# Kernel tuning notes

Measured on AMD Instinct MI355X. Metric: run time of the kernel, lower is better.

The kernel has to match this reference:

```python
import jax, jax.numpy as jnp
import numpy as np

B, T, D, H = 2, 2048, 2048, 32
HD = D // H
# quantization scales (constructor-time attributes in the original repo)
A_PROJ = 3e-4   # q/k/v proj alpha (W8A8B8O8Linear)
A_QK = 2e-5     # qk_bmm alpha (BMM_S8T_S8N_F32T)
A_PV = 1e-2     # pv_bmm alpha (BMM_S8T_S8N_S8T)
A_OUT = 1e-4    # out_proj alpha (W8A8BFP32OFP32Linear)


def _i8(key, shape):
    return jax.random.randint(key, shape, -128, 128, dtype=jnp.int32).astype(jnp.int8)


def setup_inputs() -> dict:
    key = jax.random.key(0)
    ks = jax.random.split(key, 10)
    hidden_states = _i8(ks[0], (B, T, D))
    # causal mask, 0 on/below diagonal, large negative above
    causal = jnp.triu(jnp.full((T, T), -1e9, dtype=jnp.float32), k=1)
    attention_mask = jnp.broadcast_to(causal, (B, 1, T, T))
    return {
        "hidden_states": hidden_states,
        "attention_mask": attention_mask,
        "Wq": _i8(ks[1], (D, D)), "bq": _i8(ks[2], (D,)),
        "Wk": _i8(ks[3], (D, D)), "bk": _i8(ks[4], (D,)),
        "Wv": _i8(ks[5], (D, D)), "bv": _i8(ks[6], (D,)),
        "Wo": _i8(ks[7], (D, D)),
        "bo": jax.random.normal(ks[8], (D,), dtype=jnp.float32),
    }


def _w8a8b8o8(x_i8, W_i8, b_i8, alpha):
    # int8 GEMM -> int32 accum; epilogue: alpha*acc + bias, saturate to int8
    acc = jnp.einsum('btk,nk->btn', x_i8.astype(jnp.int32), W_i8.astype(jnp.int32))
    y = alpha * acc.astype(jnp.float32) + b_i8.astype(jnp.float32)
    return jnp.clip(jnp.round(y), -128, 127).astype(jnp.int8)


def reference(hidden_states, attention_mask, Wq, bq, Wk, bk, Wv, bv, Wo, bo):
    # q/k/v projections: int8 in, int8 out
    q = _w8a8b8o8(hidden_states, Wq, bq, A_PROJ)
    k = _w8a8b8o8(hidden_states, Wk, bk, A_PROJ)
    v = _w8a8b8o8(hidden_states, Wv, bv, A_PROJ)

    def shape(x):  # [B,T,D] -> [B,H,T,HD]
        return x.reshape(B, T, H, HD).transpose(0, 2, 1, 3)

    qh, kh, vh = shape(q), shape(k), shape(v)

    # qk_bmm (BMM_S8T_S8N_F32T): fp32 = alpha * int8 q @ k^T
    attn = A_QK * jnp.einsum('bhtd,bhsd->bhts',
                             qh.astype(jnp.int32), kh.astype(jnp.int32)).astype(jnp.float32)
    attn = attn + attention_mask  # [B,1,T,T] broadcasts over heads
    attn = jnp.maximum(attn, jnp.finfo(jnp.float32).min)
    probs = jax.nn.softmax(attn, axis=-1)

    # quantize probs: p.mul_(127).round_() -> int8
    p_i8 = jnp.clip(jnp.round(probs * 127.0), -128, 127).astype(jnp.int8)

    # pv_bmm (BMM_S8T_S8N_S8T): int8 out = sat(round(alpha * p @ v))
    pv = jnp.einsum('bhts,bhsd->bhtd', p_i8.astype(jnp.int32), vh.astype(jnp.int32))
    attn_out_i8 = jnp.clip(jnp.round(A_PV * pv.astype(jnp.float32)), -128, 127).astype(jnp.int8)

    # [B,H,T,HD] -> [B,T,D]
    attn_out = attn_out_i8.transpose(0, 2, 1, 3).reshape(B, T, D)

    # out_proj (W8A8BFP32OFP32Linear): fp32 = alpha*(x@W^T) + fp32 bias
    acc = jnp.einsum('btk,nk->btn', attn_out.astype(jnp.int32), Wo.astype(jnp.int32))
    out = A_OUT * acc.astype(jnp.float32) + bo
    return out
```

## Files before the change

kernel.cpp:

```cpp
#include <hip/hip_runtime.h>
#include <cstdint>

#define A_PROJ 3e-4f
#define A_QK   2e-5f
#define A_PV   1e-2f
#define A_OUT  1e-4f

#define NB 2
#define NT 2048
#define ND 2048
#define NH 32
#define NHD 64
#define NM (NB*NT)

typedef int v4i __attribute__((ext_vector_type(4)));

__device__ __forceinline__ int8_t sat8(float y) {
  float r = rintf(y);
  r = fminf(fmaxf(r, -128.f), 127.f);
  return (int8_t)(int)r;
}

__device__ __forceinline__ float exp2_fast(float x) {
  return __builtin_amdgcn_exp2f(x);
}

__device__ __forceinline__ void gl2lds16(const int8_t* g, int8_t* l) {
  __builtin_amdgcn_global_load_lds(
      (const __attribute__((address_space(1))) void*)g,
      (__attribute__((address_space(3))) void*)l, 16, 0, 0);
}

#define NWW (ND*ND/4)
__global__ void pack_all(const int* __restrict__ X,
                         const int* __restrict__ W0, const int* __restrict__ W1,
                         const int* __restrict__ W2, const int* __restrict__ W3,
                         int8_t* __restrict__ dX, int8_t* __restrict__ dW0,
                         int8_t* __restrict__ dW1, int8_t* __restrict__ dW2,
                         int8_t* __restrict__ dW3) {
  int i = blockIdx.x * blockDim.x + threadIdx.x;
  const int nx = NM*ND/4;
  const int* src; int8_t* dst; int off;
  if (i < nx) { src = X; dst = dX; off = i; }
  else {
    int j = i - nx;
    int r = j >> 20;
    off = j & (NWW - 1);
    src = (r == 0) ? W0 : (r == 1) ? W1 : (r == 2) ? W2 : W3;
    dst = (r == 0) ? dW0 : (r == 1) ? dW1 : (r == 2) ? dW2 : dW3;
  }
  int4 v = ((const int4*)src)[off];
  uint32_t p = (uint32_t)(v.x & 255) | ((uint32_t)(v.y & 255) << 8) |
               ((uint32_t)(v.z & 255) << 16) | ((uint32_t)(v.w & 255) << 24);
  ((uint32_t*)dst)[off] = p;
}

__global__ __launch_bounds__(256) void gemm_qkv(
    const int8_t* __restrict__ X,
    const int8_t* __restrict__ Wq, const int8_t* __restrict__ Wk, const int8_t* __restrict__ Wv,
    const int* __restrict__ bq, const int* __restrict__ bk, const int* __restrict__ bv,
    int8_t* __restrict__ Qh, int8_t* __restrict__ Kh, int8_t* __restrict__ Vt)
{
  __shared__ __align__(16) int8_t As[2][128][64];
  __shared__ __align__(16) int8_t Bs[2][128][64];
  const int z = blockIdx.z;
  const int8_t* W  = (z == 0) ? Wq : ((z == 1) ? Wk : Wv);
  const int* bias  = (z == 0) ? bq : ((z == 1) ? bk : bv);
  const int m0 = blockIdx.x * 128, n0 = blockIdx.y * 128;
  const int tid = threadIdx.x, lane = tid & 63, wave = tid >> 6;
  const int wm = wave >> 1, wn = wave & 1;
  const int l15 = lane & 15, quad = lane >> 4;

  const int srow = lane >> 2;
  const int scol = (((lane & 3) ^ ((lane >> 3) & 3)) * 16);
  const int rqcol = (quad ^ ((l15 >> 1) & 3)) * 16;

  v4i acc[4][4];
  const v4i vzero = {0, 0, 0, 0};
  #pragma unroll
  for (int i = 0; i < 4; ++i)
    #pragma unroll
    for (int j = 0; j < 4; ++j) acc[i][j] = vzero;

  for (int k0 = 0; k0 < ND; k0 += 128) {
    #pragma unroll
    for (int j = 0; j < 8; ++j) {
      int slot = j * 4 + wave;
      int sl = slot & 15;
      int hh = sl >> 3, rblk = sl & 7;
      int row = rblk * 16 + srow;
      if (slot < 16) {
        gl2lds16(&X[(size_t)(m0 + row) * ND + k0 + hh * 64 + scol], &As[hh][rblk * 16][0]);
      } else {
        gl2lds16(&W[(size_t)(n0 + row) * ND + k0 + hh * 64 + scol], &Bs[hh][rblk * 16][0]);
      }
    }
    __syncthreads();
    #pragma unroll
    for (int hh = 0; hh < 2; ++hh) {
      v4i a[4], b[4];
      #pragma unroll
      for (int mt = 0; mt < 4; ++mt) a[mt] = *(const v4i*)&As[hh][wm*64 + mt*16 + l15][rqcol];
      #pragma unroll
      for (int nt = 0; nt < 4; ++nt) b[nt] = *(const v4i*)&Bs[hh][wn*64 + nt*16 + l15][rqcol];
      #pragma unroll
      for (int mt = 0; mt < 4; ++mt)
        #pragma unroll
        for (int nt = 0; nt < 4; ++nt)
          acc[mt][nt] = __builtin_amdgcn_mfma_i32_16x16x64_i8(a[mt], b[nt], acc[mt][nt], 0, 0, 0);
    }
    __syncthreads();
  }

  float bf[4];
  #pragma unroll
  for (int nt = 0; nt < 4; ++nt) bf[nt] = (float)bias[n0 + wn*64 + nt*16 + l15];

  #pragma unroll
  for (int mt = 0; mt < 4; ++mt)
    #pragma unroll
    for (int nt = 0; nt < 4; ++nt)
      #pragma unroll
      for (int r = 0; r < 4; ++r) {
        int m = m0 + wm*64 + mt*16 + quad*4 + r;
        int n = n0 + wn*64 + nt*16 + l15;
        int8_t q = sat8(A_PROJ * (float)acc[mt][nt][r] + bf[nt]);
        int bb = m >> 11, t = m & (NT - 1);
        int hd8 = n >> 6, hd = n & (NHD - 1);
        size_t bh = (size_t)bb * NH + hd8;
        if (z == 2) Vt[(bh * NHD + hd) * NT + t] = q;
        else ((z == 0) ? Qh : Kh)[(bh * NT + t) * NHD + hd] = q;
      }
}

__global__ __launch_bounds__(256) void attn_fused(
    const int8_t* __restrict__ Qh, const int8_t* __restrict__ Kh, const int8_t* __restrict__ Vt,
    int8_t* __restrict__ AO)
{
  __shared__ __align__(16) int8_t Ks[128][64];
  __shared__ __align__(16) int8_t Vs[64][128];
  __shared__ __align__(16) uint32_t Ps32[4][16][36];

  const int bx = blockIdx.x;
  const int bh = blockIdx.y;
  const int tid = threadIdx.x, lane = tid & 63, wave = tid >> 6;
  const int l15 = lane & 15, quad = lane >> 4;
  const v4i vzero = {0, 0, 0, 0};
  const float MAGIC = 12582912.0f;
  const float C2 = 2.8853900817779268e-05f;

  const int8_t* Qp = Qh + (size_t)bh * NT * NHD;
  const int8_t* Kp = Kh + (size_t)bh * NT * NHD;
  const int8_t* Vp = Vt + (size_t)bh * NHD * NT;
  const int bb = bh >> 5, hhead = bh & (NH - 1);

  const int kst_row = lane >> 2;
  const int kst_col = (((lane & 3) ^ ((lane >> 3) & 3)) * 16);
  const int vst_row = lane >> 3;
  const int vst_col = (((lane & 7) ^ ((lane >> 3) & 7)) * 16);
  const int kfcol = (quad ^ ((l15 >> 1) & 3)) * 16;

  for (int half = 0; half < 2; ++half) {
    const int xq = half ? (31 - bx) : bx;
    const int t0 = xq * 64;
    const int sd = xq >> 1;
    const int tme = t0 + wave * 16 + l15;

    v4i qf = *(const v4i*)&Qp[(size_t)(t0 + wave * 16 + l15) * NHD + quad * 16];

    float lsum = 0.f;
    for (int st = 0; st <= sd; ++st) {
      const int s0 = st * 128;
      #pragma unroll
      for (int j = 0; j < 2; ++j)
        gl2lds16(&Kp[(size_t)(s0 + j*64 + wave*16 + kst_row) * NHD + kst_col],
                 &Ks[j*64 + wave*16][0]);
      __syncthreads();
      v4i kf[8];
      #pragma unroll
      for (int mt = 0; mt < 8; ++mt) kf[mt] = *(const v4i*)&Ks[mt*16 + l15][kfcol];
      if (st < sd) {
        #pragma unroll
        for (int mt = 0; mt < 8; ++mt) {
          v4i sa = __builtin_amdgcn_mfma_i32_16x16x64_i8(kf[mt], qf, vzero, 0, 0, 0);
          #pragma unroll
          for (int r = 0; r < 4; ++r) lsum += exp2_fast(C2 * (float)sa[r]);
        }
      } else {
        #pragma unroll
        for (int mt = 0; mt < 8; ++mt) {
          v4i sa = __builtin_amdgcn_mfma_i32_16x16x64_i8(kf[mt], qf, vzero, 0, 0, 0);
          const int sbase = s0 + mt*16 + quad*4;
          #pragma unroll
          for (int r = 0; r < 4; ++r) {
            float e = exp2_fast(C2 * (float)sa[r]);
            lsum += (sbase + r <= tme) ? e : 0.f;
          }
        }
      }
      __syncthreads();
    }
    {
      lsum += __shfl_xor(lsum, 16, 64);
      lsum += __shfl_xor(lsum, 32, 64);
    }
    const float linv = 127.0f / lsum;

    v4i accv[4];
    #pragma unroll
    for (int j = 0; j < 4; ++j) accv[j] = vzero;

    for (int st = 0; st <= sd; ++st) {
      const int s0 = st * 128;
      #pragma unroll
      for (int j = 0; j < 2; ++j)
        gl2lds16(&Kp[(size_t)(s0 + j*64 + wave*16 + kst_row) * NHD + kst_col],
                 &Ks[j*64 + wave*16][0]);
      #pragma unroll
      for (int j = 0; j < 2; ++j)
        gl2lds16(&Vp[(size_t)(j*32 + wave*8 + vst_row) * NT + s0 + vst_col],
                 &Vs[j*32 + wave*8][0]);
      __syncthreads();
      v4i kf[8];
      #pragma unroll
      for (int mt = 0; mt < 8; ++mt) kf[mt] = *(const v4i*)&Ks[mt*16 + l15][kfcol];

      if (st < sd) {
        #pragma unroll
        for (int mt = 0; mt < 8; ++mt) {
          v4i sa = __builtin_amdgcn_mfma_i32_16x16x64_i8(kf[mt], qf, vzero, 0, 0, 0);
          uint32_t pk = 0;
          #pragma unroll
          for (int r = 0; r < 4; ++r) {
            float e = exp2_fast(C2 * (float)sa[r]);
            float f = fmaf(e, linv, MAGIC);
            pk |= (__float_as_uint(f) & 0xFFu) << (8 * r);
          }
          Ps32[wave][l15][mt*4 + quad] = pk;
        }
      } else {
        #pragma unroll
        for (int mt = 0; mt < 8; ++mt) {
          v4i sa = __builtin_amdgcn_mfma_i32_16x16x64_i8(kf[mt], qf, vzero, 0, 0, 0);
          uint32_t pk = 0;
          const int sbase = s0 + mt*16 + quad*4;
          #pragma unroll
          for (int r = 0; r < 4; ++r) {
            float e = (sbase + r <= tme) ? exp2_fast(C2 * (float)sa[r]) : 0.f;
            float f = fmaf(e, linv, MAGIC);
            pk |= (__float_as_uint(f) & 0xFFu) << (8 * r);
          }
          Ps32[wave][l15][mt*4 + quad] = pk;
        }
      }
      #pragma unroll
      for (int ks = 0; ks < 2; ++ks) {
        v4i ap = *(const v4i*)&Ps32[wave][l15][ks*16 + quad*4];
        #pragma unroll
        for (int nt2 = 0; nt2 < 4; ++nt2) {
          v4i bv = *(const v4i*)&Vs[nt2*16 + l15][(((ks*4 + quad) ^ (l15 & 7)) * 16)];
          accv[nt2] = __builtin_amdgcn_mfma_i32_16x16x64_i8(ap, bv, accv[nt2], 0, 0, 0);
        }
      }
      __syncthreads();
    }

    #pragma unroll
    for (int nt2 = 0; nt2 < 4; ++nt2)
      #pragma unroll
      for (int r = 0; r < 4; ++r) {
        int t = t0 + wave*16 + quad*4 + r;
        int d = nt2*16 + l15;
        AO[((size_t)bb * NT + t) * ND + hhead * NHD + d] = sat8(A_PV * (float)accv[nt2][r]);
      }
  }
}

__global__ __launch_bounds__(256) void gemm_out(
    const int8_t* __restrict__ X, const int8_t* __restrict__ W,
    const float* __restrict__ bo, float* __restrict__ out)
{
  __shared__ __align__(16) int8_t As[2][128][64];
  __shared__ __align__(16) int8_t Bs[2][128][64];
  const int m0 = blockIdx.x * 128, n0 = blockIdx.y * 128;
  const int tid = threadIdx.x, lane = tid & 63, wave = tid >> 6;
  const int wm = wave >> 1, wn = wave & 1;
  const int l15 = lane & 15, quad = lane >> 4;
  const int srow = lane >> 2;
  const int scol = (((lane & 3) ^ ((lane >> 3) & 3)) * 16);
  const int rqcol = (quad ^ ((l15 >> 1) & 3)) * 16;

  v4i acc[4][4];
  const v4i vzero = {0, 0, 0, 0};
  #pragma unroll
  for (int i = 0; i < 4; ++i)
    #pragma unroll
    for (int j = 0; j < 4; ++j) acc[i][j] = vzero;

  for (int k0 = 0; k0 < ND; k0 += 128) {
    #pragma unroll
    for (int j = 0; j < 8; ++j) {
      int slot = j * 4 + wave;
      int sl = slot & 15;
      int hh = sl >> 3, rblk = sl & 7;
      int row = rblk * 16 + srow;
      if (slot < 16) {
        gl2lds16(&X[(size_t)(m0 + row) * ND + k0 + hh * 64 + scol], &As[hh][rblk * 16][0]);
      } else {
        gl2lds16(&W[(size_t)(n0 + row) * ND + k0 + hh * 64 + scol], &Bs[hh][rblk * 16][0]);
      }
    }
    __syncthreads();
    #pragma unroll
    for (int hh = 0; hh < 2; ++hh) {
      v4i a[4], b[4];
      #pragma unroll
      for (int mt = 0; mt < 4; ++mt) a[mt] = *(const v4i*)&As[hh][wm*64 + mt*16 + l15][rqcol];
      #pragma unroll
      for (int nt = 0; nt < 4; ++nt) b[nt] = *(const v4i*)&Bs[hh][wn*64 + nt*16 + l15][rqcol];
      #pragma unroll
      for (int mt = 0; mt < 4; ++mt)
        #pragma unroll
        for (int nt = 0; nt < 4; ++nt)
          acc[mt][nt] = __builtin_amdgcn_mfma_i32_16x16x64_i8(a[mt], b[nt], acc[mt][nt], 0, 0, 0);
    }
    __syncthreads();
  }

  float bf[4];
  #pragma unroll
  for (int nt = 0; nt < 4; ++nt) bf[nt] = bo[n0 + wn*64 + nt*16 + l15];

  #pragma unroll
  for (int mt = 0; mt < 4; ++mt)
    #pragma unroll
    for (int nt = 0; nt < 4; ++nt)
      #pragma unroll
      for (int r = 0; r < 4; ++r) {
        int m = m0 + wm*64 + mt*16 + quad*4 + r;
        int n = n0 + wn*64 + nt*16 + l15;
        out[(size_t)m * ND + n] = A_OUT * (float)acc[mt][nt][r] + bf[nt];
      }
}

extern "C" void kernel_launch(void* const* d_in, const int* in_sizes, int n_in,
                              void* d_out, int out_size, void* d_ws, size_t ws_size,
                              hipStream_t stream)
{
  const int*   hs  = (const int*)d_in[0];
  const int*   Wq  = (const int*)d_in[2];
  const int*   bq  = (const int*)d_in[3];
  const int*   Wk  = (const int*)d_in[4];
  const int*   bkb = (const int*)d_in[5];
  const int*   Wv  = (const int*)d_in[6];
  const int*   bvb = (const int*)d_in[7];
  const int*   Wo  = (const int*)d_in[8];
  const float* bo  = (const float*)d_in[9];
  float* out = (float*)d_out;

  char* ws = (char*)d_ws;
  const size_t SZ_X = (size_t)NM * ND;
  const size_t SZ_W = (size_t)ND * ND;
  const size_t SZ_H = (size_t)NB * NH * NT * NHD;
  int8_t* Xp  = (int8_t*)ws;
  int8_t* Wqp = (int8_t*)(ws + SZ_X);
  int8_t* Wkp = Wqp + SZ_W;
  int8_t* Wvp = Wkp + SZ_W;
  int8_t* Wop = Wvp + SZ_W;
  int8_t* Qh  = Wop + SZ_W;
  int8_t* Kh  = Qh + SZ_H;
  int8_t* Vt  = Kh + SZ_H;
  int8_t* AO  = Xp;

  const int ntot = (int)(SZ_X/4 + 4 * (SZ_W/4));
  pack_all<<<(ntot + 255) / 256, 256, 0, stream>>>(hs, Wq, Wk, Wv, Wo,
                                                   Xp, Wqp, Wkp, Wvp, Wop);

  gemm_qkv<<<dim3(NM/128, ND/128, 3), 256, 0, stream>>>(Xp, Wqp, Wkp, Wvp, bq, bkb, bvb, Qh, Kh, Vt);
  attn_fused<<<dim3(16, NB*NH), 256, 0, stream>>>(Qh, Kh, Vt, AO);
  gemm_out<<<dim3(NM/128, ND/128), 256, 0, stream>>>(AO, Wop, bo, out);
}
```

Baseline: 336.2 us.

## Load GEMM B operand directly to registers and double-buffer A tile in LDS

New measurement: 389.2 us. 1.16x slower.

```diff
diff --git a/kernel.cpp b/kernel.cpp
--- a/kernel.cpp
+++ b/kernel.cpp
@@ -55,14 +55,13 @@
   ((uint32_t*)dst)[off] = p;
 }
 
-__global__ __launch_bounds__(256) void gemm_qkv(
+__global__ __launch_bounds__(256, 3) void gemm_qkv(
     const int8_t* __restrict__ X,
     const int8_t* __restrict__ Wq, const int8_t* __restrict__ Wk, const int8_t* __restrict__ Wv,
     const int* __restrict__ bq, const int* __restrict__ bk, const int* __restrict__ bv,
     int8_t* __restrict__ Qh, int8_t* __restrict__ Kh, int8_t* __restrict__ Vt)
 {
   __shared__ __align__(16) int8_t As[2][128][64];
-  __shared__ __align__(16) int8_t Bs[2][128][64];
   const int z = blockIdx.z;
   const int8_t* W  = (z == 0) ? Wq : ((z == 1) ? Wk : Wv);
   const int* bias  = (z == 0) ? bq : ((z == 1) ? bk : bv);
@@ -75,6 +74,13 @@
   const int scol = (((lane & 3) ^ ((lane >> 3) & 3)) * 16);
   const int rqcol = (quad ^ ((l15 >> 1) & 3)) * 16;
 
+  const int8_t* Xa0 = X + (size_t)(m0 + wave * 16 + srow) * ND + scol;
+  const int8_t* Xa1 = X + (size_t)(m0 + (wave + 4) * 16 + srow) * ND + scol;
+  int8_t* lA0[2] = { &As[0][wave * 16][0], &As[1][wave * 16][0] };
+  int8_t* lA1[2] = { &As[0][(wave + 4) * 16][0], &As[1][(wave + 4) * 16][0] };
+
+  const int8_t* Wb = W + (size_t)(n0 + wn * 64 + l15) * ND + quad * 16;
+
   v4i acc[4][4];
   const v4i vzero = {0, 0, 0, 0};
   #pragma unroll
@@ -82,55 +88,86 @@
     #pragma unroll
     for (int j = 0; j < 4; ++j) acc[i][j] = vzero;
 
+  v4i bcur[4], bnxt[4];
+  gl2lds16(Xa0, lA0[0]);
+  gl2lds16(Xa1, lA1[0]);
+  #pragma unroll
+  for (int nt = 0; nt < 4; ++nt) bcur[nt] = *(const v4i*)(Wb + (size_t)nt * 16 * ND);
+
   for (int k0 = 0; k0 < ND; k0 += 128) {
-    #pragma unroll
-    for (int j = 0; j < 8; ++j) {
-      int slot = j * 4 + wave;
-      int sl = slot & 15;
-      int hh = sl >> 3, rblk = sl & 7;
-      int row = rblk * 16 + srow;
-      if (slot < 16) {
-        gl2lds16(&X[(size_t)(m0 + row) * ND + k0 + hh * 64 + scol], &As[hh][rblk * 16][0]);
-      } else {
-        gl2lds16(&W[(size_t)(n0 + row) * ND + k0 + hh * 64 + scol], &Bs[hh][rblk * 16][0]);
-      }
-    }
     __syncthreads();
-    #pragma unroll
-    for (int hh = 0; hh < 2; ++hh) {
-      v4i a[4], b[4];
-      #pragma unroll
-      for (int mt = 0; mt < 4; ++mt) a[mt] = *(const v4i*)&As[hh][wm*64 + mt*16 + l15][rqcol];
-      #pragma unroll
-      for (int nt = 0; nt < 4; ++nt) b[nt] = *(const v4i*)&Bs[hh][wn*64 + nt*16 + l15][rqcol];
+    gl2lds16(Xa0 + k0 + 64, lA0[1]);
+    gl2lds16(Xa1 + k0 + 64, lA1[1]);
+    #pragma unroll
+    for (int nt = 0; nt < 4; ++nt) bnxt[nt] = *(const v4i*)(Wb + (size_t)nt * 16 * ND + k0 + 64);
+    {
+      v4i a[4];
+      #pragma unroll
+      for (int mt = 0; mt < 4; ++mt) a[mt] = *(const v4i*)&As[0][wm*64 + mt*16 + l15][rqcol];
       #pragma unroll
       for (int mt = 0; mt < 4; ++mt)
         #pragma unroll
         for (int nt = 0; nt < 4; ++nt)
-          acc[mt][nt] = __builtin_amdgcn_mfma_i32_16x16x64_i8(a[mt], b[nt], acc[mt][nt], 0, 0, 0);
+          acc[mt][nt] = __builtin_amdgcn_mfma_i32_16x16x64_i8(a[mt], bcur[nt], acc[mt][nt], 0, 0, 0);
     }
     __syncthreads();
+    if (k0 + 128 < ND) {
+      gl2lds16(Xa0 + k0 + 128, lA0[0]);
+      gl2lds16(Xa1 + k0 + 128, lA1[0]);
+      #pragma unroll
+      for (int nt = 0; nt < 4; ++nt) bcur[nt] = *(const v4i*)(Wb + (size_t)nt * 16 * ND + k0 + 128);
+    }
+    {
+      v4i a[4];
+      #pragma unroll
+      for (int mt = 0; mt < 4; ++mt) a[mt] = *(const v4i*)&As[1][wm*64 + mt*16 + l15][rqcol];
+      #pragma unroll
+      for (int mt = 0; mt < 4; ++mt)
+        #pragma unroll
+        for (int nt = 0; nt < 4; ++nt)
+          acc[mt][nt] = __builtin_amdgcn_mfma_i32_16x16x64_i8(a[mt], bnxt[nt], acc[mt][nt], 0, 0, 0);
+    }
   }
 
   float bf[4];
   #pragma unroll
   for (int nt = 0; nt < 4; ++nt) bf[nt] = (float)bias[n0 + wn*64 + nt*16 + l15];
 
-  #pragma unroll
-  for (int mt = 0; mt < 4; ++mt)
-    #pragma unroll
-    for (int nt = 0; nt < 4; ++nt)
-      #pragma unroll
-      for (int r = 0; r < 4; ++r) {
-        int m = m0 + wm*64 + mt*16 + quad*4 + r;
+  if (z == 2) {
+    #pragma unroll
+    for (int mt = 0; mt < 4; ++mt)
+      #pragma unroll
+      for (int nt = 0; nt < 4; ++nt) {
+        int tbase = (m0 + wm*64 + mt*16 + quad*4) & (NT - 1);
+        int bb = (m0 + wm*64) >> 11;
         int n = n0 + wn*64 + nt*16 + l15;
-        int8_t q = sat8(A_PROJ * (float)acc[mt][nt][r] + bf[nt]);
-        int bb = m >> 11, t = m & (NT - 1);
-        int hd8 = n >> 6, hd = n & (NHD - 1);
-        size_t bh = (size_t)bb * NH + hd8;
-        if (z == 2) Vt[(bh * NHD + hd) * NT + t] = q;
-        else ((z == 0) ? Qh : Kh)[(bh * NT + t) * NHD + hd] = q;
-      }
+        int hh = n >> 6, hd = n & (NHD - 1);
+        uint32_t pk = 0;
+        #pragma unroll
+        for (int r = 0; r < 4; ++r) {
+          uint32_t q = (uint32_t)(uint8_t)sat8(A_PROJ * (float)acc[mt][nt][r] + bf[nt]);
+          pk |= q << (8 * r);
+        }
+        size_t bh = (size_t)bb * NH + hh;
+        *(uint32_t*)&Vt[(bh * NHD + hd) * NT + tbase] = pk;
+      }
+  } else {
+    int8_t* O = (z == 0) ? Qh : Kh;
+    #pragma unroll
+    for (int mt = 0; mt < 4; ++mt)
+      #pragma unroll
+      for (int nt = 0; nt < 4; ++nt)
+        #pragma unroll
+        for (int r = 0; r < 4; ++r) {
+          int m = m0 + wm*64 + mt*16 + quad*4 + r;
+          int n = n0 + wn*64 + nt*16 + l15;
+          int8_t q = sat8(A_PROJ * (float)acc[mt][nt][r] + bf[nt]);
+          int bb = m >> 11, t = m & (NT - 1);
+          int hh = n >> 6, hd = n & (NHD - 1);
+          size_t bh = (size_t)bb * NH + hh;
+          O[(bh * NT + t) * NHD + hd] = q;
+        }
+  }
 }
 
 __global__ __launch_bounds__(256) void attn_fused(
@@ -276,12 +313,11 @@
   }
 }
 
-__global__ __launch_bounds__(256) void gemm_out(
+__global__ __launch_bounds__(256, 3) void gemm_out(
     const int8_t* __restrict__ X, const int8_t* __restrict__ W,
     const float* __restrict__ bo, float* __restrict__ out)
 {
   __shared__ __align__(16) int8_t As[2][128][64];
-  __shared__ __align__(16) int8_t Bs[2][128][64];
   const int m0 = blockIdx.x * 128, n0 = blockIdx.y * 128;
   const int tid = threadIdx.x, lane = tid & 63, wave = tid >> 6;
   const int wm = wave >> 1, wn = wave & 1;
@@ -290,6 +326,12 @@
   const int scol = (((lane & 3) ^ ((lane >> 3) & 3)) * 16);
   const int rqcol = (quad ^ ((l15 >> 1) & 3)) * 16;
 
+  const int8_t* Xa0 = X + (size_t)(m0 + wave * 16 + srow) * ND + scol;
+  const int8_t* Xa1 = X + (size_t)(m0 + (wave + 4) * 16 + srow) * ND + scol;
+  int8_t* lA0[2] = { &As[0][wave * 16][0], &As[1][wave * 16][0] };
+  int8_t* lA1[2] = { &As[0][(wave + 4) * 16][0], &As[1][(wave + 4) * 16][0] };
+  const int8_t* Wb = W + (size_t)(n0 + wn * 64 + l15) * ND + quad * 16;
+
   v4i acc[4][4];
   const v4i vzero = {0, 0, 0, 0};
   #pragma unroll
@@ -297,34 +339,45 @@
     #pragma unroll
     for (int j = 0; j < 4; ++j) acc[i][j] = vzero;
 
+  v4i bcur[4], bnxt[4];
+  gl2lds16(Xa0, lA0[0]);
+  gl2lds16(Xa1, lA1[0]);
+  #pragma unroll
+  for (int nt = 0; nt < 4; ++nt) bcur[nt] = *(const v4i*)(Wb + (size_t)nt * 16 * ND);
+
   for (int k0 = 0; k0 < ND; k0 += 128) {
-    #pragma unroll
-    for (int j = 0; j < 8; ++j) {
-      int slot = j * 4 + wave;
-      int sl = slot & 15;
-      int hh = sl >> 3, rblk = sl & 7;
-      int row = rblk * 16 + srow;
-      if (slot < 16) {
-        gl2lds16(&X[(size_t)(m0 + row) * ND + k0 + hh * 64 + scol], &As[hh][rblk * 16][0]);
-      } else {
-        gl2lds16(&W[(size_t)(n0 + row) * ND + k0 + hh * 64 + scol], &Bs[hh][rblk * 16][0]);
-      }
-    }
     __syncthreads();
-    #pragma unroll
-    for (int hh = 0; hh < 2; ++hh) {
-      v4i a[4], b[4];
-      #pragma unroll
-      for (int mt = 0; mt < 4; ++mt) a[mt] = *(const v4i*)&As[hh][wm*64 + mt*16 + l15][rqcol];
-      #pragma unroll
-      for (int nt = 0; nt < 4; ++nt) b[nt] = *(const v4i*)&Bs[hh][wn*64 + nt*16 + l15][rqcol];
+    gl2lds16(Xa0 + k0 + 64, lA0[1]);
+    gl2lds16(Xa1 + k0 + 64, lA1[1]);
+    #pragma unroll
+    for (int nt = 0; nt < 4; ++nt) bnxt[nt] = *(const v4i*)(Wb + (size_t)nt * 16 * ND + k0 + 64);
+    {
+      v4i a[4];
+      #pragma unroll
+      for (int mt = 0; mt < 4; ++mt) a[mt] = *(const v4i*)&As[0][wm*64 + mt*16 + l15][rqcol];
       #pragma unroll
       for (int mt = 0; mt < 4; ++mt)
         #pragma unroll
         for (int nt = 0; nt < 4; ++nt)
-          acc[mt][nt] = __builtin_amdgcn_mfma_i32_16x16x64_i8(a[mt], b[nt], acc[mt][nt], 0, 0, 0);
+          acc[mt][nt] = __builtin_amdgcn_mfma_i32_16x16x64_i8(a[mt], bcur[nt], acc[mt][nt], 0, 0, 0);
     }
     __syncthreads();
+    if (k0 + 128 < ND) {
+      gl2lds16(Xa0 + k0 + 128, lA0[0]);
+      gl2lds16(Xa1 + k0 + 128, lA1[0]);
+      #pragma unroll
+      for (int nt = 0; nt < 4; ++nt) bcur[nt] = *(const v4i*)(Wb + (size_t)nt * 16 * ND + k0 + 128);
+    }
+    {
+      v4i a[4];
+      #pragma unroll
+      for (int mt = 0; mt < 4; ++mt) a[mt] = *(const v4i*)&As[1][wm*64 + mt*16 + l15][rqcol];
+      #pragma unroll
+      for (int mt = 0; mt < 4; ++mt)
+        #pragma unroll
+        for (int nt = 0; nt < 4; ++nt)
+          acc[mt][nt] = __builtin_amdgcn_mfma_i32_16x16x64_i8(a[mt], bnxt[nt], acc[mt][nt], 0, 0, 0);
+    }
   }
 
   float bf[4];
```
